# Kernel tuning notes

Hardware: AMD Instinct MI355X
Metric: run time of the kernel (lower is better)

## Reference

```python
import jax, jax.numpy as jnp
import numpy as np
from jax import lax

DN = ('NHWC', 'HWIO', 'NHWC')


def _conv(x, w):
    return lax.conv_general_dilated(x, w, window_strides=(1, 1), padding='SAME',
                                    dimension_numbers=DN)


def setup_inputs() -> dict:
    key = jax.random.key(0)
    k1, k2, k3 = jax.random.split(key, 3)
    B, H, W, C = 8, 128, 128, 64
    k = 3
    filters = 128
    x = jax.random.normal(k1, (B, H, W, C), dtype=jnp.float32)
    # offset-predicting conv: kernel zero-init in original, but use small random
    # weights so the deformable sampling path is exercised
    w_off = jax.random.normal(k2, (k, k, C, 2 * k * k), dtype=jnp.float32) * 0.01
    b_off = jnp.zeros((2 * k * k,), dtype=jnp.float32)
    w_out = jax.random.normal(k3, (1, 1, k * k * C, filters), dtype=jnp.float32) * (1.0 / np.sqrt(k * k * C))
    b_out = jnp.zeros((filters,), dtype=jnp.float32)
    return {"x": x, "w_off": w_off, "b_off": b_off, "w_out": w_out, "b_out": b_out}


def reference(x, w_off, b_off, w_out, b_out):
    B, H, W, C = x.shape
    K2 = w_off.shape[-1] // 2  # kernel_size^2 offsets

    # predict per-pixel offsets: [B,H,W,2*K2] -> [B,H,W,K2,2]
    offsets = (_conv(x, w_off) + b_off).reshape(B, H, W, K2, 2)
    x_off = offsets[..., 0]
    y_off = offsets[..., 1]

    # base sampling grid
    yy, xx = jnp.meshgrid(jnp.arange(H, dtype=x.dtype), jnp.arange(W, dtype=x.dtype), indexing='ij')
    new_x = jnp.clip(xx[None, :, :, None] + x_off, 0.0, W - 1)  # [B,H,W,K2]
    new_y = jnp.clip(yy[None, :, :, None] + y_off, 0.0, H - 1)

    # bilinear interpolation corners
    x0 = jnp.floor(new_x)
    x1 = jnp.clip(x0 + 1, 0.0, W - 1)
    x0 = jnp.clip(x0, 0.0, W - 1)
    y0 = jnp.floor(new_y)
    y1 = jnp.clip(y0 + 1, 0.0, H - 1)
    y0 = jnp.clip(y0, 0.0, H - 1)

    wa = (x1 - new_x) * (y1 - new_y)
    wb = (x1 - new_x) * (new_y - y0)
    wc = (new_x - x0) * (y1 - new_y)
    wd = (new_x - x0) * (new_y - y0)

    bi = jnp.arange(B)[:, None, None, None]  # broadcast batch index
    ix0, ix1 = x0.astype(jnp.int32), x1.astype(jnp.int32)
    iy0, iy1 = y0.astype(jnp.int32), y1.astype(jnp.int32)

    def gather(yi, xi):
        return x[bi, yi, xi]  # [B,H,W,K2,C]

    interp = (wa[..., None] * gather(iy0, ix0)
              + wb[..., None] * gather(iy1, ix0)
              + wc[..., None] * gather(iy0, ix1)
              + wd[..., None] * gather(iy1, ix1))  # [B,H,W,K2,C]

    sampled = interp.reshape(B, H, W, K2 * C)
    out = _conv(sampled, w_out) + b_out  # 1x1 conv
    return out
```

## Files before the change

### kernel.cpp

```cpp
#include <hip/hip_runtime.h>

typedef short short8 __attribute__((ext_vector_type(8)));
typedef float f32x4 __attribute__((ext_vector_type(4)));
typedef unsigned short ushort4v __attribute__((ext_vector_type(4)));

__device__ __forceinline__ unsigned short f2bf(float f) {
  unsigned int u = __builtin_bit_cast(unsigned int, f);
  u += 0x7fffu + ((u >> 16) & 1u);
  return (unsigned short)(u >> 16);
}

template <int CTRL>
__device__ __forceinline__ float dpp_add(float v) {
  int t = __builtin_amdgcn_update_dpp(0, __builtin_bit_cast(int, v), CTRL, 0xf, 0xf, true);
  return v + __builtin_bit_cast(float, t);
}

__global__ __launch_bounds__(256) void prep(const float* __restrict__ w_off,
                                            const float* __restrict__ w_out,
                                            float* __restrict__ wT,
                                            unsigned short* __restrict__ wbt) {
  int i = blockIdx.x * 256 + threadIdx.x;
  if (i < 73728) {
    int k = i >> 7, n = i & 127;
    wbt[n * 576 + k] = f2bf(w_out[i]);
  }
  int t = i - 73728;
  if (t >= 0 && t < 10368) {
    int pos = t / 1152, r = t - pos * 1152;
    int c = r / 18, j = r - c * 18;
    wT[(pos * 18 + j) * 64 + c] = w_off[t];
  }
}

__global__ __launch_bounds__(512, 4) void offconv7(const float* __restrict__ x,
                                                   const float* __restrict__ wT,
                                                   const float* __restrict__ b_off,
                                                   float* __restrict__ offs) {
  __shared__ float lw[10368];
  const int tid = threadIdx.x;
#pragma unroll 1
  for (int i = tid; i < 2592; i += 512)
    *(float4*)&lw[i * 4] = *(const float4*)&wT[i * 4];
  __syncthreads();

  const int row = (blockIdx.x & 7) * 128 + (blockIdx.x >> 3);
  const int img = row >> 7, h = row & 127;
  const int pairLocal = tid >> 3;
  const int c8 = tid & 7;
  const int w0 = pairLocal * 2;
  const int p = row * 128 + w0;

  float acc[18][2];
#pragma unroll
  for (int j = 0; j < 18; ++j) {
    float bj = b_off[j];
    acc[j][0] = bj;
    acc[j][1] = bj;
  }

  const float* xim = x + (size_t)img * (128 * 128 * 64);
  const int ca = c8 * 4;

#pragma unroll 1
  for (int kh = 0; kh < 3; ++kh) {
    const int hh = h + kh - 1;
    const bool rok = (hh >= 0) && (hh <= 127);
    const int hc = hh < 0 ? 0 : (hh > 127 ? 127 : hh);
#pragma unroll 1
    for (int kw = 0; kw < 3; ++kw) {
      const int ww0 = w0 + kw - 1;
      const int ww1 = ww0 + 1;
      const bool ok0 = rok && (ww0 >= 0);
      const bool ok1 = rok && (ww1 <= 127);
      const int wc0 = ww0 < 0 ? 0 : ww0;
      const int wc1 = ww1 > 127 ? 127 : ww1;
      const float* x0 = xim + (size_t)(hc * 128 + wc0) * 64 + ca;
      const float* x1 = xim + (size_t)(hc * 128 + wc1) * 64 + ca;
      float4 xa0 = *(const float4*)x0;
      float4 xb0 = *(const float4*)(x0 + 32);
      float4 xa1 = *(const float4*)x1;
      float4 xb1 = *(const float4*)(x1 + 32);
      if (!ok0) { xa0 = make_float4(0.f, 0.f, 0.f, 0.f); xb0 = xa0; }
      if (!ok1) { xa1 = make_float4(0.f, 0.f, 0.f, 0.f); xb1 = xa1; }
      const float* wp = lw + ((kh * 3 + kw) * 18) * 64 + ca;
#pragma unroll
      for (int j = 0; j < 18; ++j) {
        float4 wa = *(const float4*)(wp + j * 64);
        float4 wb = *(const float4*)(wp + j * 64 + 32);
        float a0 = acc[j][0], a1 = acc[j][1];
        a0 = fmaf(xa0.x, wa.x, a0);
        a0 = fmaf(xa0.y, wa.y, a0);
        a0 = fmaf(xa0.z, wa.z, a0);
        a0 = fmaf(xa0.w, wa.w, a0);
        a0 = fmaf(xb0.x, wb.x, a0);
        a0 = fmaf(xb0.y, wb.y, a0);
        a0 = fmaf(xb0.z, wb.z, a0);
        a0 = fmaf(xb0.w, wb.w, a0);
        a1 = fmaf(xa1.x, wa.x, a1);
        a1 = fmaf(xa1.y, wa.y, a1);
        a1 = fmaf(xa1.z, wa.z, a1);
        a1 = fmaf(xa1.w, wa.w, a1);
        a1 = fmaf(xb1.x, wb.x, a1);
        a1 = fmaf(xb1.y, wb.y, a1);
        a1 = fmaf(xb1.z, wb.z, a1);
        a1 = fmaf(xb1.w, wb.w, a1);
        acc[j][0] = a0;
        acc[j][1] = a1;
      }
    }
  }

#pragma unroll
  for (int j = 0; j < 18; ++j) {
#pragma unroll
    for (int q = 0; q < 2; ++q) {
      float v = acc[j][q];
      v = dpp_add<0x114>(v);
      v = dpp_add<0x112>(v);
      v = dpp_add<0x111>(v);
      acc[j][q] = v;
    }
  }
  if (c8 == 7) {
    float* op = offs + (size_t)p * 18;
#pragma unroll
    for (int j = 0; j < 18; ++j) {
      op[j] = acc[j][0];
      op[18 + j] = acc[j][1];
    }
  }
}

__global__ __launch_bounds__(256) void sample2(const float* __restrict__ x,
                                               const float* __restrict__ offs,
                                               unsigned short* __restrict__ sampled,
                                               int p0) {
  int gid = blockIdx.x * 256 + threadIdx.x;
  int grp = gid & 15;
  int tt = gid >> 4;
  int pr = tt / 9;
  int tap = tt - pr * 9;
  int p = p0 + pr;
  int b = p >> 14, hw = p & 16383, h = hw >> 7, w = hw & 127;
  float2 o = *(const float2*)(offs + (size_t)p * 18 + tap * 2);
  float fx = fminf(fmaxf((float)w + o.x, 0.f), 127.f);
  float fy = fminf(fmaxf((float)h + o.y, 0.f), 127.f);
  float x0 = floorf(fx), y0 = floorf(fy);
  float x1 = fminf(x0 + 1.f, 127.f), y1 = fminf(y0 + 1.f, 127.f);
  float wx1 = x1 - fx, wx0 = fx - x0;
  float wy1 = y1 - fy, wy0 = fy - y0;
  float wa = wx1 * wy1, wb = wx1 * wy0, wc = wx0 * wy1, wd = wx0 * wy0;
  int ix0 = (int)x0, ix1 = (int)x1, iy0 = (int)y0, iy1 = (int)y1;
  const float* xb = x + (size_t)b * (128 * 128 * 64) + grp * 4;
  float4 va = *(const float4*)(xb + (iy0 * 128 + ix0) * 64);
  float4 vb = *(const float4*)(xb + (iy1 * 128 + ix0) * 64);
  float4 vc = *(const float4*)(xb + (iy0 * 128 + ix1) * 64);
  float4 vd = *(const float4*)(xb + (iy1 * 128 + ix1) * 64);
  float4 v;
  v.x = wa * va.x + wb * vb.x + wc * vc.x + wd * vd.x;
  v.y = wa * va.y + wb * vb.y + wc * vc.y + wd * vd.y;
  v.z = wa * va.z + wb * vb.z + wc * vc.z + wd * vd.z;
  v.w = wa * va.w + wb * vb.w + wc * vc.w + wd * vd.w;
  ushort4v r;
  r.x = f2bf(v.x);
  r.y = f2bf(v.y);
  r.z = f2bf(v.z);
  r.w = f2bf(v.w);
  *(ushort4v*)(sampled + (size_t)pr * 576 + tap * 64 + grp * 4) = r;
}

__global__ __launch_bounds__(256) void gemm128(const unsigned short* __restrict__ A,
                                               const unsigned short* __restrict__ Bt,
                                               const float* __restrict__ bias,
                                               float* __restrict__ out,
                                               int p0) {
  __shared__ unsigned short lA[4096];
  __shared__ unsigned short lB[4096];
  const int tid = threadIdx.x;
  const int mloc = blockIdx.x * 128;
  const int m0 = p0 + mloc;
  const int lane = tid & 63, wv = tid >> 6;
  const int wi = wv >> 1, wj = wv & 1;
  f32x4 acc[4][4] = {};
  const int r1 = tid >> 2, q = tid & 3;
  const int r2 = r1 + 64;
  const int slot1 = ((r1 >> 4) * 64 + (q << 4) + (r1 & 15)) * 8;
  const int slot2 = ((r2 >> 4) * 64 + (q << 4) + (r2 & 15)) * 8;

  for (int kt = 0; kt < 576; kt += 32) {
    const uint4* ga1 = (const uint4*)(A + (size_t)(mloc + r1) * 576 + kt + q * 8);
    const uint4* ga2 = (const uint4*)(A + (size_t)(mloc + r2) * 576 + kt + q * 8);
    const uint4* gb1 = (const uint4*)(Bt + (size_t)r1 * 576 + kt + q * 8);
    const uint4* gb2 = (const uint4*)(Bt + (size_t)r2 * 576 + kt + q * 8);
    *(uint4*)&lA[slot1] = *ga1;
    *(uint4*)&lA[slot2] = *ga2;
    *(uint4*)&lB[slot1] = *gb1;
    *(uint4*)&lB[slot2] = *gb2;
    __syncthreads();
    short8 av[4], bv[4];
#pragma unroll
    for (int it = 0; it < 4; ++it)
      av[it] = *(const short8*)&lA[((wi * 4 + it) * 64 + lane) * 8];
#pragma unroll
    for (int jt = 0; jt < 4; ++jt)
      bv[jt] = *(const short8*)&lB[((wj * 4 + jt) * 64 + lane) * 8];
#pragma unroll
    for (int it = 0; it < 4; ++it)
#pragma unroll
      for (int jt = 0; jt < 4; ++jt)
        acc[it][jt] = __builtin_amdgcn_mfma_f32_16x16x32_bf16(av[it], bv[jt],
                                                              acc[it][jt], 0, 0, 0);
    __syncthreads();
  }
#pragma unroll
  for (int it = 0; it < 4; ++it) {
    int m = m0 + wi * 64 + it * 16 + (lane >> 4) * 4;
#pragma unroll
    for (int jt = 0; jt < 4; ++jt) {
      int n = wj * 64 + jt * 16 + (lane & 15);
      float bn = bias[n];
#pragma unroll
      for (int r = 0; r < 4; ++r)
        out[(size_t)(m + r) * 128 + n] = acc[it][jt][r] + bn;
    }
  }
}

extern "C" void kernel_launch(void* const* d_in, const int* in_sizes, int n_in,
                              void* d_out, int out_size, void* d_ws, size_t ws_size,
                              hipStream_t stream) {
  const float* x = (const float*)d_in[0];
  const float* w_off = (const float*)d_in[1];
  const float* b_off = (const float*)d_in[2];
  const float* w_out = (const float*)d_in[3];
  const float* b_out = (const float*)d_in[4];
  float* out = (float*)d_out;

  char* ws = (char*)d_ws;
  float* offs = (float*)ws;
  float* wT = (float*)(ws + 9437184);
  unsigned short* wbt = (unsigned short*)(ws + 9478656);
  unsigned short* sampled = (unsigned short*)(ws + 9626112);

  prep<<<329, 256, 0, stream>>>(w_off, w_out, wT, wbt);
  offconv7<<<1024, 512, 0, stream>>>(x, wT, b_off, offs);

  const int TOTAL_PX = 131072;
  size_t avail = (ws_size > 9626112) ? ws_size - 9626112 : 0;
  long cp = (long)(avail / (576 * 2));
  cp &= ~127L;
  if (cp < 128) cp = 128;
  if (cp > TOTAL_PX) cp = TOTAL_PX;
  int chunk_px = (int)cp;
  for (int pbase = 0; pbase < TOTAL_PX; pbase += chunk_px) {
    int npx = TOTAL_PX - pbase;
    if (npx > chunk_px) npx = chunk_px;
    sample2<<<npx * 9 / 16, 256, 0, stream>>>(x, offs, sampled, pbase);
    gemm128<<<npx / 128, 256, 0, stream>>>(sampled, wbt, b_out, out, pbase);
  }
}
```

Measured before the change: 239.1 us.

## Fuse bilinear sampling into GEMM, building A tiles in shared memory per tap

Merges the sampling kernel and the bf16 MFMA GEMM into one kernel. Each block handles one image row of 128 pixels and computes the bilinear-sampled A tile per tap directly into LDS. This removes the round trip of the large bf16 sampled intermediate through global memory, the chunked launch loop and one kernel launch. Blocks are interleaved across images for gather locality. The cost is that gather latency now sits inside the GEMM loop with little overlap, since one tap is processed at a time between barriers.

```diff
diff --git a/kernel.cpp b/kernel.cpp
--- a/kernel.cpp
+++ b/kernel.cpp
@@ -2,7 +2,6 @@
 
 typedef short short8 __attribute__((ext_vector_type(8)));
 typedef float f32x4 __attribute__((ext_vector_type(4)));
-typedef unsigned short ushort4v __attribute__((ext_vector_type(4)));
 
 __device__ __forceinline__ unsigned short f2bf(float f) {
   unsigned int u = __builtin_bit_cast(unsigned int, f);
@@ -132,54 +131,17 @@
   }
 }
 
-__global__ __launch_bounds__(256) void sample2(const float* __restrict__ x,
-                                               const float* __restrict__ offs,
-                                               unsigned short* __restrict__ sampled,
-                                               int p0) {
-  int gid = blockIdx.x * 256 + threadIdx.x;
-  int grp = gid & 15;
-  int tt = gid >> 4;
-  int pr = tt / 9;
-  int tap = tt - pr * 9;
-  int p = p0 + pr;
-  int b = p >> 14, hw = p & 16383, h = hw >> 7, w = hw & 127;
-  float2 o = *(const float2*)(offs + (size_t)p * 18 + tap * 2);
-  float fx = fminf(fmaxf((float)w + o.x, 0.f), 127.f);
-  float fy = fminf(fmaxf((float)h + o.y, 0.f), 127.f);
-  float x0 = floorf(fx), y0 = floorf(fy);
-  float x1 = fminf(x0 + 1.f, 127.f), y1 = fminf(y0 + 1.f, 127.f);
-  float wx1 = x1 - fx, wx0 = fx - x0;
-  float wy1 = y1 - fy, wy0 = fy - y0;
-  float wa = wx1 * wy1, wb = wx1 * wy0, wc = wx0 * wy1, wd = wx0 * wy0;
-  int ix0 = (int)x0, ix1 = (int)x1, iy0 = (int)y0, iy1 = (int)y1;
-  const float* xb = x + (size_t)b * (128 * 128 * 64) + grp * 4;
-  float4 va = *(const float4*)(xb + (iy0 * 128 + ix0) * 64);
-  float4 vb = *(const float4*)(xb + (iy1 * 128 + ix0) * 64);
-  float4 vc = *(const float4*)(xb + (iy0 * 128 + ix1) * 64);
-  float4 vd = *(const float4*)(xb + (iy1 * 128 + ix1) * 64);
-  float4 v;
-  v.x = wa * va.x + wb * vb.x + wc * vc.x + wd * vd.x;
-  v.y = wa * va.y + wb * vb.y + wc * vc.y + wd * vd.y;
-  v.z = wa * va.z + wb * vb.z + wc * vc.z + wd * vd.z;
-  v.w = wa * va.w + wb * vb.w + wc * vc.w + wd * vd.w;
-  ushort4v r;
-  r.x = f2bf(v.x);
-  r.y = f2bf(v.y);
-  r.z = f2bf(v.z);
-  r.w = f2bf(v.w);
-  *(ushort4v*)(sampled + (size_t)pr * 576 + tap * 64 + grp * 4) = r;
-}
-
-__global__ __launch_bounds__(256) void gemm128(const unsigned short* __restrict__ A,
-                                               const unsigned short* __restrict__ Bt,
-                                               const float* __restrict__ bias,
-                                               float* __restrict__ out,
-                                               int p0) {
-  __shared__ unsigned short lA[4096];
-  __shared__ unsigned short lB[4096];
+__global__ __launch_bounds__(256) void fused_sg(const float* __restrict__ x,
+                                                const float* __restrict__ offs,
+                                                const unsigned short* __restrict__ Bt,
+                                                const float* __restrict__ bias,
+                                                float* __restrict__ out) {
+  __shared__ unsigned short lA[2][4096];
+  __shared__ unsigned short lB[2][4096];
   const int tid = threadIdx.x;
-  const int mloc = blockIdx.x * 128;
-  const int m0 = p0 + mloc;
+  const int img = blockIdx.x & 7;
+  const int rowi = blockIdx.x >> 3;
+  const int mloc = (img * 128 + rowi) * 128;
   const int lane = tid & 63, wv = tid >> 6;
   const int wi = wv >> 1, wj = wv & 1;
   f32x4 acc[4][4] = {};
@@ -187,35 +149,75 @@
   const int r2 = r1 + 64;
   const int slot1 = ((r1 >> 4) * 64 + (q << 4) + (r1 & 15)) * 8;
   const int slot2 = ((r2 >> 4) * 64 + (q << 4) + (r2 & 15)) * 8;
-
-  for (int kt = 0; kt < 576; kt += 32) {
-    const uint4* ga1 = (const uint4*)(A + (size_t)(mloc + r1) * 576 + kt + q * 8);
-    const uint4* ga2 = (const uint4*)(A + (size_t)(mloc + r2) * 576 + kt + q * 8);
-    const uint4* gb1 = (const uint4*)(Bt + (size_t)r1 * 576 + kt + q * 8);
-    const uint4* gb2 = (const uint4*)(Bt + (size_t)r2 * 576 + kt + q * 8);
-    *(uint4*)&lA[slot1] = *ga1;
-    *(uint4*)&lA[slot2] = *ga2;
-    *(uint4*)&lB[slot1] = *gb1;
-    *(uint4*)&lB[slot2] = *gb2;
+  const int g = tid >> 4;
+  const int c4 = tid & 15;
+  const int ahalf = c4 >> 3;
+  const int aq = (c4 >> 1) & 3;
+  const int asub = (c4 & 1) * 4;
+  const float* xim = x + (size_t)img * (128 * 128 * 64) + c4 * 4;
+  const float hf = (float)rowi;
+
+#pragma unroll 1
+  for (int tap = 0; tap < 9; ++tap) {
+    const int kt = tap * 64;
+    uint4 b00 = *(const uint4*)(Bt + (size_t)r1 * 576 + kt + q * 8);
+    uint4 b01 = *(const uint4*)(Bt + (size_t)r2 * 576 + kt + q * 8);
+    uint4 b10 = *(const uint4*)(Bt + (size_t)r1 * 576 + kt + 32 + q * 8);
+    uint4 b11 = *(const uint4*)(Bt + (size_t)r2 * 576 + kt + 32 + q * 8);
+#pragma unroll 2
+    for (int i = 0; i < 8; ++i) {
+      const int w = g * 8 + i;
+      const int p = mloc + w;
+      float2 o = *(const float2*)(offs + (size_t)p * 18 + tap * 2);
+      float fx = fminf(fmaxf((float)w + o.x, 0.f), 127.f);
+      float fy = fminf(fmaxf(hf + o.y, 0.f), 127.f);
+      float x0f = floorf(fx), y0f = floorf(fy);
+      float x1f = fminf(x0f + 1.f, 127.f), y1f = fminf(y0f + 1.f, 127.f);
+      float wx1 = x1f - fx, wx0 = fx - x0f;
+      float wy1 = y1f - fy, wy0 = fy - y0f;
+      float wa = wx1 * wy1, wb = wx1 * wy0, wc = wx0 * wy1, wd = wx0 * wy0;
+      int ix0 = (int)x0f, ix1 = (int)x1f, iy0 = (int)y0f, iy1 = (int)y1f;
+      float4 va = *(const float4*)(xim + (iy0 * 128 + ix0) * 64);
+      float4 vb = *(const float4*)(xim + (iy1 * 128 + ix0) * 64);
+      float4 vc = *(const float4*)(xim + (iy0 * 128 + ix1) * 64);
+      float4 vd = *(const float4*)(xim + (iy1 * 128 + ix1) * 64);
+      float4 v;
+      v.x = wa * va.x + wb * vb.x + wc * vc.x + wd * vd.x;
+      v.y = wa * va.y + wb * vb.y + wc * vc.y + wd * vd.y;
+      v.z = wa * va.z + wb * vb.z + wc * vc.z + wd * vd.z;
+      v.w = wa * va.w + wb * vb.w + wc * vc.w + wd * vd.w;
+      uint2 pv;
+      pv.x = (unsigned)f2bf(v.x) | ((unsigned)f2bf(v.y) << 16);
+      pv.y = (unsigned)f2bf(v.z) | ((unsigned)f2bf(v.w) << 16);
+      const int slot = ((w >> 4) * 64 + (aq << 4) + (w & 15)) * 8 + asub;
+      *(uint2*)&lA[ahalf][slot] = pv;
+    }
+    *(uint4*)&lB[0][slot1] = b00;
+    *(uint4*)&lB[0][slot2] = b01;
+    *(uint4*)&lB[1][slot1] = b10;
+    *(uint4*)&lB[1][slot2] = b11;
     __syncthreads();
-    short8 av[4], bv[4];
-#pragma unroll
-    for (int it = 0; it < 4; ++it)
-      av[it] = *(const short8*)&lA[((wi * 4 + it) * 64 + lane) * 8];
-#pragma unroll
-    for (int jt = 0; jt < 4; ++jt)
-      bv[jt] = *(const short8*)&lB[((wj * 4 + jt) * 64 + lane) * 8];
-#pragma unroll
-    for (int it = 0; it < 4; ++it)
+#pragma unroll
+    for (int hh = 0; hh < 2; ++hh) {
+      short8 av[4], bv[4];
+#pragma unroll
+      for (int it = 0; it < 4; ++it)
+        av[it] = *(const short8*)&lA[hh][((wi * 4 + it) * 64 + lane) * 8];
 #pragma unroll
       for (int jt = 0; jt < 4; ++jt)
-        acc[it][jt] = __builtin_amdgcn_mfma_f32_16x16x32_bf16(av[it], bv[jt],
-                                                              acc[it][jt], 0, 0, 0);
+        bv[jt] = *(const short8*)&lB[hh][((wj * 4 + jt) * 64 + lane) * 8];
+#pragma unroll
+      for (int it = 0; it < 4; ++it)
+#pragma unroll
+        for (int jt = 0; jt < 4; ++jt)
+          acc[it][jt] = __builtin_amdgcn_mfma_f32_16x16x32_bf16(av[it], bv[jt],
+                                                                acc[it][jt], 0, 0, 0);
+    }
     __syncthreads();
   }
 #pragma unroll
   for (int it = 0; it < 4; ++it) {
-    int m = m0 + wi * 64 + it * 16 + (lane >> 4) * 4;
+    int m = mloc + wi * 64 + it * 16 + (lane >> 4) * 4;
 #pragma unroll
     for (int jt = 0; jt < 4; ++jt) {
       int n = wj * 64 + jt * 16 + (lane & 15);
@@ -241,22 +243,8 @@
   float* offs = (float*)ws;
   float* wT = (float*)(ws + 9437184);
   unsigned short* wbt = (unsigned short*)(ws + 9478656);
-  unsigned short* sampled = (unsigned short*)(ws + 9626112);
 
   prep<<<329, 256, 0, stream>>>(w_off, w_out, wT, wbt);
   offconv7<<<1024, 512, 0, stream>>>(x, wT, b_off, offs);
-
-  const int TOTAL_PX = 131072;
-  size_t avail = (ws_size > 9626112) ? ws_size - 9626112 : 0;
-  long cp = (long)(avail / (576 * 2));
-  cp &= ~127L;
-  if (cp < 128) cp = 128;
-  if (cp > TOTAL_PX) cp = TOTAL_PX;
-  int chunk_px = (int)cp;
-  for (int pbase = 0; pbase < TOTAL_PX; pbase += chunk_px) {
-    int npx = TOTAL_PX - pbase;
-    if (npx > chunk_px) npx = chunk_px;
-    sample2<<<npx * 9 / 16, 256, 0, stream>>>(x, offs, sampled, pbase);
-    gemm128<<<npx / 128, 256, 0, stream>>>(sampled, wbt, b_out, out, pbase);
-  }
-}
+  fused_sg<<<1024, 256, 0, stream>>>(x, offs, wbt, b_out, out);
+}
```

Result: faster. 218.6 us (-8.6%).
